# Kernel optimization log

Measured on AMD Instinct MI355X. Metric: run time of the kernel, lower is better.

## Reference

```python
import jax, jax.numpy as jnp
import numpy as np

D_MODEL = 1024
N_HEADS = 16
D_K = D_MODEL // N_HEADS


def setup_inputs() -> dict:
    key = jax.random.key(0)
    ks = jax.random.split(key, 9)
    B, S, D = 2, 2048, D_MODEL
    q = jax.random.normal(ks[0], (B, S, D), dtype=jnp.float32)
    v = jax.random.normal(ks[1], (B, S, D), dtype=jnp.float32)
    k = jax.random.normal(ks[2], (B, S, D), dtype=jnp.float32)
    att_mask = jnp.zeros((B, S, S), dtype=jnp.float32)
    seq_mask = jax.random.uniform(ks[3], (B, S, S), dtype=jnp.float32)
    scale = 1.0 / np.sqrt(D)
    Wq = jax.random.normal(ks[4], (D, D), dtype=jnp.float32) * scale
    Wk = jax.random.normal(ks[5], (D, D), dtype=jnp.float32) * scale
    Wv = jax.random.normal(ks[6], (D, D), dtype=jnp.float32) * scale
    Wo = jax.random.normal(ks[7], (D, D), dtype=jnp.float32) * scale
    return {"q": q, "v": v, "k": k, "att_mask": att_mask, "seq_mask": seq_mask,
            "Wq": Wq, "Wk": Wk, "Wv": Wv, "Wo": Wo}


def _split_heads(x, B):
    # [B, S, D] -> [B, H, S, d_k]
    return x.reshape(B, -1, N_HEADS, D_K).transpose(0, 2, 1, 3)


def reference(q, v, k, att_mask, seq_mask, Wq, Wk, Wv, Wo):
    B = q.shape[0]
    qh = _split_heads(q @ Wq, B)
    kh = _split_heads(k @ Wk, B)
    vh = _split_heads(v @ Wv, B)
    # scores: [B, H, Sq, Sk]
    scores = jnp.einsum('bhqd,bhkd->bhqk', qh, kh) / jnp.sqrt(jnp.float32(D_K))
    scores = scores + att_mask[:, None]
    attn = jax.nn.softmax(scores, axis=-1)
    attn = attn * seq_mask[:, None]  # post-softmax multiplicative mask
    out = jnp.einsum('bhqk,bhkd->bhqd', attn, vh)
    out = out.transpose(0, 2, 1, 3).reshape(B, -1, D_MODEL)
    return out @ Wo
```

## Files before the change

kernel.cpp:

```cpp
#include <hip/hip_runtime.h>
#include <cstddef>

typedef __attribute__((ext_vector_type(8))) short s16x8;
typedef __attribute__((ext_vector_type(4))) float f32x4;
typedef __attribute__((ext_vector_type(4))) unsigned short us4;

static __device__ __forceinline__ float bf2f(unsigned short u) {
    union { unsigned u; float f; } v;
    v.u = ((unsigned)u) << 16;
    return v.f;
}

static __device__ __forceinline__ unsigned short f2bf(float f) {
    union { float f; unsigned u; } v;
    v.f = f;
    unsigned r = v.u + 0x7fffu + ((v.u >> 16) & 1u);
    return (unsigned short)(r >> 16);
}

static __device__ __forceinline__ unsigned short f2bf_fast(float f) {
    unsigned r;
    asm("v_cvt_pk_bf16_f32 %0, %1, %2" : "=v"(r) : "v"(f), "v"(f));
    return (unsigned short)r;
}

#if __has_builtin(__builtin_amdgcn_exp2f)
#define EXP2F(x) __builtin_amdgcn_exp2f(x)
#else
#define EXP2F(x) exp2f(x)
#endif

typedef const __attribute__((address_space(1))) unsigned int* as1_cu32p;
typedef __attribute__((address_space(3))) unsigned int* as3_u32p;
static __device__ __forceinline__ void async16(const void* g, void* l) {
    __builtin_amdgcn_global_load_lds((as1_cu32p)g, (as3_u32p)l, 16, 0, 0);
}

static __device__ __forceinline__ float ldf(const unsigned short* p, size_t i) { return bf2f(p[i]); }
static __device__ __forceinline__ float ldf(const float* p, size_t i) { return p[i]; }
static __device__ __forceinline__ void stf(unsigned short* p, size_t i, float v) { p[i] = f2bf(v); }
static __device__ __forceinline__ void stf(float* p, size_t i, float v) { p[i] = v; }

__global__ __launch_bounds__(256) void probe_dtype(
    const unsigned short* __restrict__ q, unsigned* __restrict__ flags)
{
    __shared__ float red[256];
    const int t = threadIdx.x;
    float m = 0.0f;
    for (int i = t; i < 16384; i += 256) {
        float x = fabsf(bf2f(q[i]));
        if (!(x == x)) x = 1.0e30f;
        m = fmaxf(m, x);
    }
    red[t] = m;
    __syncthreads();
    for (int s = 128; s > 0; s >>= 1) {
        if (t < s) red[t] = fmaxf(red[t], red[t + s]);
        __syncthreads();
    }
    if (t == 0) {
        flags[0] = (red[0] < 1000.0f) ? 0u : 1u;
        flags[1] = 0u;
    }
}

__global__ __launch_bounds__(256) void probe_zero(
    const uint4* __restrict__ m, unsigned* __restrict__ flags)
{
    const unsigned dt = flags[0];
    const size_t n = dt ? 2097152u : 1048576u;
    unsigned acc = 0;
    for (size_t i = (size_t)blockIdx.x * 256 + threadIdx.x; i < n;
         i += (size_t)gridDim.x * 256) {
        uint4 v = m[i];
        acc |= v.x | v.y | v.z | v.w;
    }
    if (acc) atomicOr(&flags[1], 1u);
}

__global__ __launch_bounds__(256) void cvt3_f32_bf16(
    const float4* __restrict__ s0, us4* __restrict__ d0,
    const float4* __restrict__ s1, us4* __restrict__ d1,
    const float4* __restrict__ s2, us4* __restrict__ d2,
    unsigned n4, const unsigned* __restrict__ flags)
{
    if (flags[0] != 1u) return;
    const float4* s = (blockIdx.y == 0) ? s0 : (blockIdx.y == 1) ? s1 : s2;
    us4* d = (blockIdx.y == 0) ? d0 : (blockIdx.y == 1) ? d1 : d2;
    for (unsigned i = blockIdx.x * 256u + threadIdx.x; i < n4;
         i += gridDim.x * 256u) {
        float4 v = s[i];
        us4 o;
        o.x = f2bf(v.x); o.y = f2bf(v.y); o.z = f2bf(v.z); o.w = f2bf(v.w);
        d[i] = o;
    }
}

__global__ __launch_bounds__(256) void cvt_f32_bf16(
    const float4* __restrict__ src, us4* __restrict__ dst, unsigned n4,
    const unsigned* __restrict__ flags)
{
    if (flags[0] != 1u) return;
    for (unsigned i = blockIdx.x * 256u + threadIdx.x; i < n4;
         i += gridDim.x * 256u) {
        float4 v = src[i];
        us4 o;
        o.x = f2bf(v.x); o.y = f2bf(v.y); o.z = f2bf(v.z); o.w = f2bf(v.w);
        dst[i] = o;
    }
}

template <typename T>
__global__ __launch_bounds__(256) void transpose_w4(
    const T* __restrict__ s0, const T* __restrict__ s1, const T* __restrict__ s2,
    const T* __restrict__ s3, unsigned short* __restrict__ dst4,
    const unsigned* __restrict__ flag, unsigned want)
{
    if (*flag != want) return;
    const int z = blockIdx.z;
    const T* src = (z == 0) ? s0 : (z == 1) ? s1 : (z == 2) ? s2 : s3;
    unsigned short* dst = dst4 + (size_t)z * 1024 * 1024;
    __shared__ unsigned short tile[32][33];
    const int c0 = blockIdx.x * 32, r0 = blockIdx.y * 32;
    const int tx = threadIdx.x, ty = threadIdx.y;
#pragma unroll
    for (int i = 0; i < 32; i += 8)
        tile[ty + i][tx] = f2bf(ldf(src, (size_t)(r0 + ty + i) * 1024 + c0 + tx));
    __syncthreads();
#pragma unroll
    for (int i = 0; i < 32; i += 8)
        dst[(size_t)(c0 + ty + i) * 1024 + r0 + tx] = tile[tx][ty + i];
}

template <typename TO>
static __device__ __forceinline__ void gemm128_body(
    const unsigned short* __restrict__ A, const unsigned short* __restrict__ Bt,
    TO* __restrict__ out, int mode, int m0, int n0)
{
    const int K = 1024;
    __shared__ __align__(16) unsigned short lA[2][128 * 64];
    __shared__ __align__(16) unsigned short lB[2][128 * 64];

    const int t = threadIdx.x;
    const int w = t >> 6, l = t & 63, quad = l >> 4, l15 = l & 15;
    const int wr = w >> 1, wc = w & 1;

    const int srow = t >> 3;
    const int scol = (((t & 7) ^ ((t >> 3) & 7)) * 8);
    const unsigned short* Asrc = A + (size_t)(m0 + srow) * K + scol;
    const unsigned short* Bsrc = Bt + (size_t)(n0 + srow) * K + scol;

    f32x4 acc[4][4] = {};

#pragma unroll
    for (int n = 0; n < 4; n++) {
        async16(Asrc + (size_t)(n * 32) * K, (char*)&lA[0][0] + w * 1024 + n * 4096);
        async16(Bsrc + (size_t)(n * 32) * K, (char*)&lB[0][0] + w * 1024 + n * 4096);
    }

    int cur = 0;
    for (int k0 = 0; k0 < K; k0 += 64) {
        __syncthreads();
        if (k0 + 64 < K) {
            char* da = (char*)&lA[cur ^ 1][0] + w * 1024;
            char* db = (char*)&lB[cur ^ 1][0] + w * 1024;
#pragma unroll
            for (int n = 0; n < 4; n++) {
                async16(Asrc + (size_t)(n * 32) * K + (k0 + 64), da + n * 4096);
                async16(Bsrc + (size_t)(n * 32) * K + (k0 + 64), db + n * 4096);
            }
        }
        const unsigned short* pA = &lA[cur][0];
        const unsigned short* pB = &lB[cur][0];
        const int sw = (l15 & 7) * 8;
#pragma unroll
        for (int kk = 0; kk < 64; kk += 32) {
            const int co = (kk + quad * 8) ^ sw;
            s16x8 af[4], bf[4];
#pragma unroll
            for (int i = 0; i < 4; i++)
                af[i] = *(const s16x8*)&pA[(wr * 64 + i * 16 + l15) * 64 + co];
#pragma unroll
            for (int j = 0; j < 4; j++)
                bf[j] = *(const s16x8*)&pB[(wc * 64 + j * 16 + l15) * 64 + co];
#pragma unroll
            for (int i = 0; i < 4; i++)
#pragma unroll
                for (int j = 0; j < 4; j++)
                    acc[i][j] = __builtin_amdgcn_mfma_f32_16x16x32_bf16(
                        af[i], bf[j], acc[i][j], 0, 0, 0);
        }
        cur ^= 1;
    }

#pragma unroll
    for (int i = 0; i < 4; i++) {
#pragma unroll
        for (int j = 0; j < 4; j++) {
#pragma unroll
            for (int r = 0; r < 4; r++) {
                int row = m0 + wr * 64 + i * 16 + quad * 4 + r;
                int col = n0 + wc * 64 + j * 16 + l15;
                float val = acc[i][j][r];
                if (mode == 0) {
                    stf(out, (size_t)row * 1024 + col, val);
                } else {
                    int b = row >> 11, s = row & 2047;
                    int h = col >> 6, d = col & 63;
                    if (mode == 1)
                        stf(out, (((size_t)(b * 16 + h) * 2048) + s) * 64 + d, val);
                    else
                        stf(out, (((size_t)(b * 16 + h) * 64) + d) * 2048 + s, val);
                }
            }
        }
    }
}

__global__ __launch_bounds__(256) void gemm3_kernel(
    const unsigned short* __restrict__ q0, const unsigned short* __restrict__ k0,
    const unsigned short* __restrict__ v0, const unsigned short* __restrict__ qb,
    const unsigned short* __restrict__ kb, const unsigned short* __restrict__ vb,
    const unsigned short* __restrict__ wt, unsigned short* __restrict__ qh,
    unsigned short* __restrict__ kh, unsigned short* __restrict__ vt,
    const unsigned* __restrict__ flags)
{
    const int z = blockIdx.z;
    const bool f = (flags[0] != 0u);
    const unsigned short* A = (z == 0) ? (f ? qb : q0)
                            : (z == 1) ? (f ? kb : k0) : (f ? vb : v0);
    const unsigned short* Bt = wt + (size_t)z * 1024 * 1024;
    unsigned short* out = (z == 0) ? qh : (z == 1) ? kh : vt;
    gemm128_body<unsigned short>(A, Bt, out, (z == 2) ? 2 : 1,
                                 blockIdx.y * 128, blockIdx.x * 128);
}

__global__ __launch_bounds__(256) void gemm_out_kernel(
    const unsigned short* __restrict__ A, const unsigned short* __restrict__ Bt,
    void* __restrict__ out, const unsigned* __restrict__ flags)
{
    if (flags[0] != 0u)
        gemm128_body<float>(A, Bt, (float*)out, 0, blockIdx.y * 128, blockIdx.x * 128);
    else
        gemm128_body<unsigned short>(A, Bt, (unsigned short*)out, 0,
                                     blockIdx.y * 128, blockIdx.x * 128);
}

__global__ __launch_bounds__(256) void attn_kernel(
    const unsigned short* __restrict__ qh, const unsigned short* __restrict__ kh,
    const unsigned short* __restrict__ vt, const void* __restrict__ amaskv,
    const unsigned short* __restrict__ sm_bf, const unsigned short* __restrict__ sm_raw,
    unsigned short* __restrict__ aout, const unsigned* __restrict__ flags)
{
    const bool isf32 = (flags[0] != 0u);
    const bool useA = (flags[1] != 0u);
    const int S = 2048, DK = 64, H = 16;
    const int qt = blockIdx.x, h = blockIdx.y, b = blockIdx.z;
    const unsigned short* qhb = qh + (size_t)(b * H + h) * S * DK;
    const unsigned short* khb = kh + (size_t)(b * H + h) * S * DK;
    const unsigned short* vtb = vt + (size_t)(b * H + h) * DK * S;
    const unsigned short* smask = isf32 ? sm_bf : sm_raw;
    const unsigned short* smb = smask + (size_t)b * S * S;

    __shared__ __align__(16) unsigned short lK[64 * 64];
    __shared__ __align__(16) unsigned short lM[64 * 64];
    __shared__ __align__(16) unsigned short lV[2][64 * 64];
    __shared__ __align__(16) unsigned short lP[4][16 * 64];

    const int t = threadIdx.x;
    const int w = t >> 6, l = t & 63, quad = l >> 4, l15 = l & 15;
    const int q0 = qt * 64;

    const float SCALE2 = 0.18033688011112042f;
    const float LOG2E  = 1.4426950408889634f;

    const int trow = t >> 3;
    const int tcol = (((t & 7) ^ ((t >> 3) & 7)) * 8);
    const unsigned short* ksrc0 = khb + (size_t)trow * DK + tcol;
    const unsigned short* ksrc1 = khb + (size_t)(trow + 32) * DK + tcol;
    const unsigned short* msrc0 = smb + (size_t)(q0 + trow) * S + tcol;
    const unsigned short* msrc1 = smb + (size_t)(q0 + trow + 32) * S + tcol;
    const unsigned short* vsrc0 = vtb + (size_t)trow * S + tcol;
    const unsigned short* vsrc1 = vtb + (size_t)(trow + 32) * S + tcol;
    char* kdst = (char*)lK + (t >> 6) * 1024;
    char* mdst = (char*)lM + (t >> 6) * 1024;
    char* vbase = (char*)&lV[0][0] + (t >> 6) * 1024;

    async16(ksrc0, kdst); async16(ksrc1, kdst + 4096);
    async16(msrc0, mdst); async16(msrc1, mdst + 4096);
    async16(vsrc0, vbase); async16(vsrc1, vbase + 4096);

    const int ksw = (l15 & 7) * 8;

    const int qrow_a = q0 + w * 16 + l15;
    s16x8 qf0 = *(const s16x8*)&qhb[(size_t)qrow_a * DK + quad * 8];
    s16x8 qf1 = *(const s16x8*)&qhb[(size_t)qrow_a * DK + 32 + quad * 8];

    float lsum[4];
    f32x4 o[4] = {};
#pragma unroll
    for (int r = 0; r < 4; r++) lsum[r] = 0.0f;

    if (!useA) {
        int it = 0;
        for (int k0 = 0; k0 < S; k0 += 64, ++it) {
            __syncthreads();

            f32x4 sc[4] = {};
#pragma unroll
            for (int kk = 0; kk < 64; kk += 32) {
                s16x8 af = (kk == 0) ? qf0 : qf1;
#pragma unroll
                for (int g = 0; g < 4; g++) {
                    s16x8 bf = *(const s16x8*)&lK[(g * 16 + l15) * 64 + ((kk + quad * 8) ^ ksw)];
                    sc[g] = __builtin_amdgcn_mfma_f32_16x16x32_bf16(af, bf, sc[g], 0, 0, 0);
                }
            }

#pragma unroll
            for (int r = 0; r < 4; r++) {
                float e0 = EXP2F(fminf(sc[0][r] * SCALE2, 100.0f));
                float e1 = EXP2F(fminf(sc[1][r] * SCALE2, 100.0f));
                float e2 = EXP2F(fminf(sc[2][r] * SCALE2, 100.0f));
                float e3 = EXP2F(fminf(sc[3][r] * SCALE2, 100.0f));
                lsum[r] += (e0 + e1) + (e2 + e3);
                const int rowp = quad * 4 + r;
                const int rowm = (w * 16 + rowp) * 64;
                const int msw = (rowp & 7) * 8;
                lP[w][rowp * 64 + ((0 * 16 + l15) ^ msw)] = f2bf_fast(e0 * bf2f(lM[rowm + ((0 * 16 + l15) ^ msw)]));
                lP[w][rowp * 64 + ((1 * 16 + l15) ^ msw)] = f2bf_fast(e1 * bf2f(lM[rowm + ((1 * 16 + l15) ^ msw)]));
                lP[w][rowp * 64 + ((2 * 16 + l15) ^ msw)] = f2bf_fast(e2 * bf2f(lM[rowm + ((2 * 16 + l15) ^ msw)]));
                lP[w][rowp * 64 + ((3 * 16 + l15) ^ msw)] = f2bf_fast(e3 * bf2f(lM[rowm + ((3 * 16 + l15) ^ msw)]));
            }
            __syncthreads();

            const int kn = (k0 + 64) & (S - 1);
            if (kn) {
                async16(ksrc0 + (size_t)kn * DK, kdst);
                async16(ksrc1 + (size_t)kn * DK, kdst + 4096);
                async16(msrc0 + kn, mdst);
                async16(msrc1 + kn, mdst + 4096);
                char* vd = vbase + ((it + 1) & 1) * 8192;
                async16(vsrc0 + kn, vd);
                async16(vsrc1 + kn, vd + 4096);
            }

            const unsigned short* lVc = &lV[it & 1][0];
#pragma unroll
            for (int kk = 0; kk < 64; kk += 32) {
                s16x8 pf = *(const s16x8*)&lP[w][l15 * 64 + ((kk + quad * 8) ^ ksw)];
#pragma unroll
                for (int g = 0; g < 4; g++) {
                    s16x8 vf = *(const s16x8*)&lVc[(g * 16 + l15) * 64 + ((kk + quad * 8) ^ ksw)];
                    o[g] = __builtin_amdgcn_mfma_f32_16x16x32_bf16(pf, vf, o[g], 0, 0, 0);
                }
            }
        }
    } else {
        const float* amf = (const float*)amaskv + (size_t)b * S * S;
        const unsigned short* amu = (const unsigned short*)amaskv + (size_t)b * S * S;
        float mrun[4];
#pragma unroll
        for (int r = 0; r < 4; r++) mrun[r] = -INFINITY;
        int it = 0;
        for (int k0 = 0; k0 < S; k0 += 64, ++it) {
            __syncthreads();

            f32x4 sc[4] = {};
#pragma unroll
            for (int kk = 0; kk < 64; kk += 32) {
                s16x8 af = (kk == 0) ? qf0 : qf1;
#pragma unroll
                for (int g = 0; g < 4; g++) {
                    s16x8 bf = *(const s16x8*)&lK[(g * 16 + l15) * 64 + ((kk + quad * 8) ^ ksw)];
                    sc[g] = __builtin_amdgcn_mfma_f32_16x16x32_bf16(af, bf, sc[g], 0, 0, 0);
                }
            }

#pragma unroll
            for (int r = 0; r < 4; r++) {
                const size_t mrow = (size_t)(q0 + w * 16 + quad * 4 + r) * S + k0;
                float a0, a1, a2, a3;
                if (isf32) {
                    a0 = amf[mrow + 0 * 16 + l15]; a1 = amf[mrow + 1 * 16 + l15];
                    a2 = amf[mrow + 2 * 16 + l15]; a3 = amf[mrow + 3 * 16 + l15];
                } else {
                    a0 = bf2f(amu[mrow + 0 * 16 + l15]); a1 = bf2f(amu[mrow + 1 * 16 + l15]);
                    a2 = bf2f(amu[mrow + 2 * 16 + l15]); a3 = bf2f(amu[mrow + 3 * 16 + l15]);
                }
                float sv0 = fmaf(a0, LOG2E, sc[0][r] * SCALE2);
                float sv1 = fmaf(a1, LOG2E, sc[1][r] * SCALE2);
                float sv2 = fmaf(a2, LOG2E, sc[2][r] * SCALE2);
                float sv3 = fmaf(a3, LOG2E, sc[3][r] * SCALE2);
                float mx = fmaxf(fmaxf(sv0, sv1), fmaxf(sv2, sv3));
#pragma unroll
                for (int d = 1; d < 16; d <<= 1) mx = fmaxf(mx, __shfl_xor(mx, d));
                float mnew = fmaxf(mrun[r], mx);
                float alpha = EXP2F(mrun[r] - mnew);
                float e0 = EXP2F(sv0 - mnew);
                float e1 = EXP2F(sv1 - mnew);
                float e2 = EXP2F(sv2 - mnew);
                float e3 = EXP2F(sv3 - mnew);
                lsum[r] = lsum[r] * alpha + ((e0 + e1) + (e2 + e3));
                mrun[r] = mnew;
#pragma unroll
                for (int g = 0; g < 4; g++) o[g][r] *= alpha;
                const int rowp = quad * 4 + r;
                const int rowm = (w * 16 + rowp) * 64;
                const int msw = (rowp & 7) * 8;
                lP[w][rowp * 64 + ((0 * 16 + l15) ^ msw)] = f2bf_fast(e0 * bf2f(lM[rowm + ((0 * 16 + l15) ^ msw)]));
                lP[w][rowp * 64 + ((1 * 16 + l15) ^ msw)] = f2bf_fast(e1 * bf2f(lM[rowm + ((1 * 16 + l15) ^ msw)]));
                lP[w][rowp * 64 + ((2 * 16 + l15) ^ msw)] = f2bf_fast(e2 * bf2f(lM[rowm + ((2 * 16 + l15) ^ msw)]));
                lP[w][rowp * 64 + ((3 * 16 + l15) ^ msw)] = f2bf_fast(e3 * bf2f(lM[rowm + ((3 * 16 + l15) ^ msw)]));
            }
            __syncthreads();

            const int kn = (k0 + 64) & (S - 1);
            if (kn) {
                async16(ksrc0 + (size_t)kn * DK, kdst);
                async16(ksrc1 + (size_t)kn * DK, kdst + 4096);
                async16(msrc0 + kn, mdst);
                async16(msrc1 + kn, mdst + 4096);
                char* vd = vbase + ((it + 1) & 1) * 8192;
                async16(vsrc0 + kn, vd);
                async16(vsrc1 + kn, vd + 4096);
            }

            const unsigned short* lVc = &lV[it & 1][0];
#pragma unroll
            for (int kk = 0; kk < 64; kk += 32) {
                s16x8 pf = *(const s16x8*)&lP[w][l15 * 64 + ((kk + quad * 8) ^ ksw)];
#pragma unroll
                for (int g = 0; g < 4; g++) {
                    s16x8 vf = *(const s16x8*)&lVc[(g * 16 + l15) * 64 + ((kk + quad * 8) ^ ksw)];
                    o[g] = __builtin_amdgcn_mfma_f32_16x16x32_bf16(pf, vf, o[g], 0, 0, 0);
                }
            }
        }
    }

#pragma unroll
    for (int r = 0; r < 4; r++) {
        float ls = lsum[r];
#pragma unroll
        for (int d = 1; d < 16; d <<= 1) ls += __shfl_xor(ls, d);
        float inv = 1.0f / ls;
        const int qr = q0 + w * 16 + quad * 4 + r;
#pragma unroll
        for (int g = 0; g < 4; g++) {
            aout[((size_t)(b * S + qr)) * 1024 + h * 64 + g * 16 + l15] =
                f2bf_fast(o[g][r] * inv);
        }
    }
}

extern "C" void kernel_launch(void* const* d_in, const int* in_sizes, int n_in,
                              void* d_out, int out_size, void* d_ws, size_t ws_size,
                              hipStream_t stream)
{
    const void* q   = d_in[0];
    const void* v   = d_in[1];
    const void* k   = d_in[2];
    const void* att = d_in[3];
    const void* seq = d_in[4];
    const void* Wq  = d_in[5];
    const void* Wk  = d_in[6];
    const void* Wv  = d_in[7];
    const void* Wo  = d_in[8];

    const size_t WELEM = 1024 * 1024;
    const size_t HELEM = (size_t)2 * 16 * 2048 * 64;

    unsigned* flags = (unsigned*)d_ws;
    unsigned short* base = (unsigned short*)((char*)d_ws + 512);
    unsigned short* wt = base;
    unsigned short* qh = wt + 4 * WELEM;
    unsigned short* kh = qh + HELEM;
    unsigned short* vt = kh + HELEM;
    unsigned short* qb = vt + HELEM;
    unsigned short* kb = qb + HELEM;
    unsigned short* vb = kb + HELEM;
    unsigned short* seqb = qb;
    unsigned short* ao = vb;

    const dim3 tw4(32, 32, 4), tb(32, 8);
    const dim3 gg(8, 32), gb(256);
    const dim3 gg3(8, 32, 3);
    const dim3 ag(32, 16, 2), ab(256);

    probe_dtype<<<1, 256, 0, stream>>>((const unsigned short*)q, flags);
    probe_zero<<<1024, 256, 0, stream>>>((const uint4*)att, flags);

    cvt3_f32_bf16<<<dim3(512, 3), 256, 0, stream>>>(
        (const float4*)q, (us4*)qb, (const float4*)k, (us4*)kb,
        (const float4*)v, (us4*)vb, 1048576u, flags);

    transpose_w4<unsigned short><<<tw4, tb, 0, stream>>>(
        (const unsigned short*)Wq, (const unsigned short*)Wk,
        (const unsigned short*)Wv, (const unsigned short*)Wo, wt, flags, 0);
    transpose_w4<float><<<tw4, tb, 0, stream>>>(
        (const float*)Wq, (const float*)Wk, (const float*)Wv, (const float*)Wo,
        wt, flags, 1);

    gemm3_kernel<<<gg3, gb, 0, stream>>>(
        (const unsigned short*)q, (const unsigned short*)k, (const unsigned short*)v,
        qb, kb, vb, wt, qh, kh, vt, flags);

    cvt_f32_bf16<<<2048, 256, 0, stream>>>((const float4*)seq, (us4*)seqb, 2097152u, flags);

    attn_kernel<<<ag, ab, 0, stream>>>(
        qh, kh, vt, att, seqb, (const unsigned short*)seq, ao, flags);

    gemm_out_kernel<<<gg, gb, 0, stream>>>(ao, wt + 3 * WELEM, d_out, flags);
}
```

Baseline: 379.5 us.

## Double-buffer K tiles, prefetch K/V at loop top, pad P buffer

K gets a second shared-memory buffer, and the next K and V tiles are now issued at the start of each iteration, so their loads overlap the QK^T, softmax and PV work. The mask tile still loads after the mid-loop barrier because it has only one buffer. The P staging buffer moves from an XOR swizzle to a row stride of 72 elements, which simplifies addressing and is meant to avoid LDS bank conflicts. The cost is more LDS per block, which may lower occupancy, and the correctness of the async-copy wait ordering now depends on the new prefetch position.

```diff
diff --git a/kernel.cpp b/kernel.cpp
--- a/kernel.cpp
+++ b/kernel.cpp
@@ -262,10 +262,10 @@
     const unsigned short* smask = isf32 ? sm_bf : sm_raw;
     const unsigned short* smb = smask + (size_t)b * S * S;
 
-    __shared__ __align__(16) unsigned short lK[64 * 64];
+    __shared__ __align__(16) unsigned short lK[2][64 * 64];
     __shared__ __align__(16) unsigned short lM[64 * 64];
     __shared__ __align__(16) unsigned short lV[2][64 * 64];
-    __shared__ __align__(16) unsigned short lP[4][16 * 64];
+    __shared__ __align__(16) unsigned short lP[4][16 * 72];
 
     const int t = threadIdx.x;
     const int w = t >> 6, l = t & 63, quad = l >> 4, l15 = l & 15;
@@ -282,12 +282,12 @@
     const unsigned short* msrc1 = smb + (size_t)(q0 + trow + 32) * S + tcol;
     const unsigned short* vsrc0 = vtb + (size_t)trow * S + tcol;
     const unsigned short* vsrc1 = vtb + (size_t)(trow + 32) * S + tcol;
-    char* kdst = (char*)lK + (t >> 6) * 1024;
-    char* mdst = (char*)lM + (t >> 6) * 1024;
-    char* vbase = (char*)&lV[0][0] + (t >> 6) * 1024;
-
-    async16(ksrc0, kdst); async16(ksrc1, kdst + 4096);
-    async16(msrc0, mdst); async16(msrc1, mdst + 4096);
+    char* kbase = (char*)&lK[0][0] + w * 1024;
+    char* mdst  = (char*)lM + w * 1024;
+    char* vbase = (char*)&lV[0][0] + w * 1024;
+
+    async16(ksrc0, kbase); async16(ksrc1, kbase + 4096);
+    async16(msrc0, mdst);  async16(msrc1, mdst + 4096);
     async16(vsrc0, vbase); async16(vsrc1, vbase + 4096);
 
     const int ksw = (l15 & 7) * 8;
@@ -305,14 +305,25 @@
         int it = 0;
         for (int k0 = 0; k0 < S; k0 += 64, ++it) {
             __syncthreads();
-
+            const int kn = (k0 + 64) & (S - 1);
+            const int cur = it & 1, nxt = (it + 1) & 1;
+            if (kn) {
+                char* kd = kbase + nxt * 8192;
+                async16(ksrc0 + (size_t)kn * DK, kd);
+                async16(ksrc1 + (size_t)kn * DK, kd + 4096);
+                char* vd = vbase + nxt * 8192;
+                async16(vsrc0 + kn, vd);
+                async16(vsrc1 + kn, vd + 4096);
+            }
+
+            const unsigned short* lKc = &lK[cur][0];
             f32x4 sc[4] = {};
 #pragma unroll
             for (int kk = 0; kk < 64; kk += 32) {
                 s16x8 af = (kk == 0) ? qf0 : qf1;
 #pragma unroll
                 for (int g = 0; g < 4; g++) {
-                    s16x8 bf = *(const s16x8*)&lK[(g * 16 + l15) * 64 + ((kk + quad * 8) ^ ksw)];
+                    s16x8 bf = *(const s16x8*)&lKc[(g * 16 + l15) * 64 + ((kk + quad * 8) ^ ksw)];
                     sc[g] = __builtin_amdgcn_mfma_f32_16x16x32_bf16(af, bf, sc[g], 0, 0, 0);
                 }
             }
@@ -327,28 +338,22 @@
                 const int rowp = quad * 4 + r;
                 const int rowm = (w * 16 + rowp) * 64;
                 const int msw = (rowp & 7) * 8;
-                lP[w][rowp * 64 + ((0 * 16 + l15) ^ msw)] = f2bf_fast(e0 * bf2f(lM[rowm + ((0 * 16 + l15) ^ msw)]));
-                lP[w][rowp * 64 + ((1 * 16 + l15) ^ msw)] = f2bf_fast(e1 * bf2f(lM[rowm + ((1 * 16 + l15) ^ msw)]));
-                lP[w][rowp * 64 + ((2 * 16 + l15) ^ msw)] = f2bf_fast(e2 * bf2f(lM[rowm + ((2 * 16 + l15) ^ msw)]));
-                lP[w][rowp * 64 + ((3 * 16 + l15) ^ msw)] = f2bf_fast(e3 * bf2f(lM[rowm + ((3 * 16 + l15) ^ msw)]));
+                lP[w][rowp * 72 + 0 * 16 + l15] = f2bf_fast(e0 * bf2f(lM[rowm + ((0 * 16 + l15) ^ msw)]));
+                lP[w][rowp * 72 + 1 * 16 + l15] = f2bf_fast(e1 * bf2f(lM[rowm + ((1 * 16 + l15) ^ msw)]));
+                lP[w][rowp * 72 + 2 * 16 + l15] = f2bf_fast(e2 * bf2f(lM[rowm + ((2 * 16 + l15) ^ msw)]));
+                lP[w][rowp * 72 + 3 * 16 + l15] = f2bf_fast(e3 * bf2f(lM[rowm + ((3 * 16 + l15) ^ msw)]));
             }
             __syncthreads();
 
-            const int kn = (k0 + 64) & (S - 1);
             if (kn) {
-                async16(ksrc0 + (size_t)kn * DK, kdst);
-                async16(ksrc1 + (size_t)kn * DK, kdst + 4096);
                 async16(msrc0 + kn, mdst);
                 async16(msrc1 + kn, mdst + 4096);
-                char* vd = vbase + ((it + 1) & 1) * 8192;
-                async16(vsrc0 + kn, vd);
-                async16(vsrc1 + kn, vd + 4096);
-            }
-
-            const unsigned short* lVc = &lV[it & 1][0];
+            }
+
+            const unsigned short* lVc = &lV[cur][0];
 #pragma unroll
             for (int kk = 0; kk < 64; kk += 32) {
-                s16x8 pf = *(const s16x8*)&lP[w][l15 * 64 + ((kk + quad * 8) ^ ksw)];
+                s16x8 pf = *(const s16x8*)&lP[w][l15 * 72 + kk + quad * 8];
 #pragma unroll
                 for (int g = 0; g < 4; g++) {
                     s16x8 vf = *(const s16x8*)&lVc[(g * 16 + l15) * 64 + ((kk + quad * 8) ^ ksw)];
@@ -365,14 +370,25 @@
         int it = 0;
         for (int k0 = 0; k0 < S; k0 += 64, ++it) {
             __syncthreads();
-
+            const int kn = (k0 + 64) & (S - 1);
+            const int cur = it & 1, nxt = (it + 1) & 1;
+            if (kn) {
+                char* kd = kbase + nxt * 8192;
+                async16(ksrc0 + (size_t)kn * DK, kd);
+                async16(ksrc1 + (size_t)kn * DK, kd + 4096);
+                char* vd = vbase + nxt * 8192;
+                async16(vsrc0 + kn, vd);
+                async16(vsrc1 + kn, vd + 4096);
+            }
+
+            const unsigned short* lKc = &lK[cur][0];
             f32x4 sc[4] = {};
 #pragma unroll
             for (int kk = 0; kk < 64; kk += 32) {
                 s16x8 af = (kk == 0) ? qf0 : qf1;
 #pragma unroll
                 for (int g = 0; g < 4; g++) {
-                    s16x8 bf = *(const s16x8*)&lK[(g * 16 + l15) * 64 + ((kk + quad * 8) ^ ksw)];
+                    s16x8 bf = *(const s16x8*)&lKc[(g * 16 + l15) * 64 + ((kk + quad * 8) ^ ksw)];
                     sc[g] = __builtin_amdgcn_mfma_f32_16x16x32_bf16(af, bf, sc[g], 0, 0, 0);
                 }
             }
@@ -408,28 +424,22 @@
                 const int rowp = quad * 4 + r;
                 const int rowm = (w * 16 + rowp) * 64;
                 const int msw = (rowp & 7) * 8;
-                lP[w][rowp * 64 + ((0 * 16 + l15) ^ msw)] = f2bf_fast(e0 * bf2f(lM[rowm + ((0 * 16 + l15) ^ msw)]));
-                lP[w][rowp * 64 + ((1 * 16 + l15) ^ msw)] = f2bf_fast(e1 * bf2f(lM[rowm + ((1 * 16 + l15) ^ msw)]));
-                lP[w][rowp * 64 + ((2 * 16 + l15) ^ msw)] = f2bf_fast(e2 * bf2f(lM[rowm + ((2 * 16 + l15) ^ msw)]));
-                lP[w][rowp * 64 + ((3 * 16 + l15) ^ msw)] = f2bf_fast(e3 * bf2f(lM[rowm + ((3 * 16 + l15) ^ msw)]));
+                lP[w][rowp * 72 + 0 * 16 + l15] = f2bf_fast(e0 * bf2f(lM[rowm + ((0 * 16 + l15) ^ msw)]));
+                lP[w][rowp * 72 + 1 * 16 + l15] = f2bf_fast(e1 * bf2f(lM[rowm + ((1 * 16 + l15) ^ msw)]));
+                lP[w][rowp * 72 + 2 * 16 + l15] = f2bf_fast(e2 * bf2f(lM[rowm + ((2 * 16 + l15) ^ msw)]));
+                lP[w][rowp * 72 + 3 * 16 + l15] = f2bf_fast(e3 * bf2f(lM[rowm + ((3 * 16 + l15) ^ msw)]));
             }
             __syncthreads();
 
-            const int kn = (k0 + 64) & (S - 1);
             if (kn) {
-                async16(ksrc0 + (size_t)kn * DK, kdst);
-                async16(ksrc1 + (size_t)kn * DK, kdst + 4096);
                 async16(msrc0 + kn, mdst);
                 async16(msrc1 + kn, mdst + 4096);
-                char* vd = vbase + ((it + 1) & 1) * 8192;
-                async16(vsrc0 + kn, vd);
-                async16(vsrc1 + kn, vd + 4096);
-            }
-
-            const unsigned short* lVc = &lV[it & 1][0];
+            }
+
+            const unsigned short* lVc = &lV[cur][0];
 #pragma unroll
             for (int kk = 0; kk < 64; kk += 32) {
-                s16x8 pf = *(const s16x8*)&lP[w][l15 * 64 + ((kk + quad * 8) ^ ksw)];
+                s16x8 pf = *(const s16x8*)&lP[w][l15 * 72 + kk + quad * 8];
 #pragma unroll
                 for (int g = 0; g < 4; g++) {
                     s16x8 vf = *(const s16x8*)&lVc[(g * 16 + l15) * 64 + ((kk + quad * 8) ^ ksw)];
```

Result: faster. 366.2 us (-3.5%).
